# Kernel tuning notes

Measured on AMD Instinct MI355X. Metric: run time of the kernel, lower is better.

## Reference

```python
import jax, jax.numpy as jnp
import numpy as np

N = 50000        # nodes
E = 1_600_000    # edges (avg degree 32)
D_IN = 128
D_H = 128
D_OUT = 128


def expmap0(x):
    # Poincare ball (c=1): expmap0(v) = tanh(||v||) * v / ||v||
    n = jnp.maximum(jnp.linalg.norm(x, axis=-1, keepdims=True), 1e-15)
    return jnp.tanh(n) * x / n


def gat_layer(x, src, dst, W, a_src, a_dst, b, n_nodes):
    # PyG GATConv, heads=1: h = xW; e_ij = LeakyReLU(a_src.h_j + a_dst.h_i);
    # softmax over incoming edges of each target i; out_i = sum_j alpha_ij h_j + b
    h = x @ W                                   # [N, d_out]
    s = h @ a_src                               # [N]
    d = h @ a_dst                               # [N]
    e = jax.nn.leaky_relu(s[src] + d[dst], 0.2)  # [E']
    m = jax.ops.segment_max(e, dst, num_segments=n_nodes)
    num = jnp.exp(e - m[dst])
    den = jax.ops.segment_sum(num, dst, num_segments=n_nodes)
    alpha = num / den[dst]                      # [E']
    out = jax.ops.segment_sum(alpha[:, None] * h[src], dst, num_segments=n_nodes)
    return out + b


def setup_inputs() -> dict:
    key = jax.random.key(0)
    ks = jax.random.split(key, 16)
    p = lambda k, shape: (jax.random.normal(k, shape, jnp.float32) * 0.08)
    inp = {
        "x": jax.random.normal(ks[0], (N, D_IN), jnp.float32),
        "edge_index": jax.random.randint(ks[1], (2, E), 0, N, dtype=jnp.int64)
        if jax.config.jax_enable_x64 else jax.random.randint(ks[1], (2, E), 0, N, dtype=jnp.int32),
        "W1": p(ks[2], (D_IN, D_H)),  "a1s": p(ks[3], (D_H,)), "a1d": p(ks[4], (D_H,)), "b1": jnp.zeros((D_H,), jnp.float32),
        "W2": p(ks[5], (D_H, D_H)),   "a2s": p(ks[6], (D_H,)), "a2d": p(ks[7], (D_H,)), "b2": jnp.zeros((D_H,), jnp.float32),
        "W3": p(ks[8], (D_H, D_OUT)), "a3s": p(ks[9], (D_OUT,)), "a3d": p(ks[10], (D_OUT,)), "b3": jnp.zeros((D_OUT,), jnp.float32),
    }
    return inp


def reference(x, edge_index, W1, a1s, a1d, b1, W2, a2s, a2d, b2, W3, a3s, a3d, b3):
    # add self loops (PyG GATConv default)
    loop = jnp.arange(N, dtype=edge_index.dtype)
    src = jnp.concatenate([edge_index[0], loop])
    dst = jnp.concatenate([edge_index[1], loop])
    h = expmap0(x)
    h = jnp.tanh(gat_layer(h, src, dst, W1, a1s, a1d, b1, N)) * 2
    # dropout(p=0.2) is identity in eval mode
    h = jnp.tanh(gat_layer(h, src, dst, W2, a2s, a2d, b2, N)) * 2
    return gat_layer(h, src, dst, W3, a3s, a3d, b3, N)
```

## Files before the change

kernel.cpp:

```cpp
#include <hip/hip_runtime.h>
#include <math.h>

#define D 128
#define CAP 80

typedef __attribute__((ext_vector_type(8))) short short8;
typedef __attribute__((ext_vector_type(4))) float float4v;
typedef __attribute__((ext_vector_type(4))) _Float16 half4v;

__device__ __forceinline__ unsigned short f2bf(float x) {
    unsigned u = __float_as_uint(x);
    u += ((u >> 16) & 1u) + 0x7fffu;
    return (unsigned short)(u >> 16);
}
__device__ __forceinline__ float bf2f(unsigned short h) {
    return __uint_as_float((unsigned)h << 16);
}


__global__ void k_prep(const float* __restrict__ W0, const float* __restrict__ W1,
                       const float* __restrict__ W2, unsigned short* __restrict__ whi,
                       unsigned short* __restrict__ wlo, int* __restrict__ cnt, int N) {
    int id = blockIdx.x * blockDim.x + threadIdx.x;
    if (id < 6144) {
        int l = id >> 11;
        int id2 = id & 2047;
        const float* W = (l == 0) ? W0 : (l == 1) ? W1 : W2;
        int lane = id2 & 63;
        int tile = id2 >> 6;
        int kt = tile & 3;
        int ct = tile >> 2;
        int k0 = kt * 32 + (lane >> 4) * 8;
        int n  = ct * 16 + (lane & 15);
        size_t base = (size_t)l * 16384 + (size_t)id2 * 8;
        for (int j = 0; j < 8; j++) {
            float w = W[(k0 + j) * D + n];
            unsigned short h = f2bf(w);
            whi[base + j] = h;
            wlo[base + j] = f2bf(w - bf2f(h));
        }
    } else {
        int i = id - 6144;
        if (i < N) cnt[i] = 0;
    }
}


__global__ void k_fill(const int* __restrict__ ei, int E, int N, int* __restrict__ cnt,
                       int* __restrict__ bucket) {
    int part = blockIdx.x & 7;
    int slice = blockIdx.x >> 3;
    int nsl = gridDim.x >> 3;
    int lo = (int)((long long)N * part >> 3);
    int hi = (int)((long long)N * (part + 1) >> 3);
    const int* dst = ei + E;
    for (int i = slice * blockDim.x + threadIdx.x; i < E; i += nsl * blockDim.x) {
        int d_ = dst[i];
        if (d_ >= lo && d_ < hi) {
            int s_ = ei[i];
            int p = atomicAdd(&cnt[d_], 1);
            if (p < CAP) bucket[(size_t)d_ * CAP + p] = s_;
        }
    }
}


template <bool EXP>
__device__ __forceinline__ void prep_frags(const float* __restrict__ A, int rg, int N,
                                           int quad, short8* bhi, short8* blo) {
    bool valid = rg < N;
    const float* arow = &A[(size_t)(valid ? rg : 0) * D];
    float af[32];
#pragma unroll
    for (int kt = 0; kt < 4; kt++) {
        int k0 = kt * 32 + quad * 8;
        float4 x0 = valid ? *(const float4*)&arow[k0]     : make_float4(0.f, 0.f, 0.f, 0.f);
        float4 x1 = valid ? *(const float4*)&arow[k0 + 4] : make_float4(0.f, 0.f, 0.f, 0.f);
        af[kt * 8 + 0] = x0.x; af[kt * 8 + 1] = x0.y; af[kt * 8 + 2] = x0.z; af[kt * 8 + 3] = x0.w;
        af[kt * 8 + 4] = x1.x; af[kt * 8 + 5] = x1.y; af[kt * 8 + 6] = x1.z; af[kt * 8 + 7] = x1.w;
    }
    if (EXP) {
        float ss = 0.f;
#pragma unroll
        for (int q = 0; q < 32; q++) ss += af[q] * af[q];
        ss += __shfl_xor(ss, 16, 64);
        ss += __shfl_xor(ss, 32, 64);
        float n = fmaxf(sqrtf(ss), 1e-15f);
        float sc = tanhf(n) / n;
#pragma unroll
        for (int q = 0; q < 32; q++) af[q] *= sc;
    }
#pragma unroll
    for (int kt = 0; kt < 4; kt++) {
#pragma unroll
        for (int j = 0; j < 8; j++) {
            float v = af[kt * 8 + j];
            unsigned short h = f2bf(v);
            bhi[kt][j] = (short)h;
            blo[kt][j] = (short)f2bf(v - bf2f(h));
        }
    }
}


template <bool EXP>
__global__ __launch_bounds__(256) void k_gemm(const float* __restrict__ A,
                                              const unsigned short* __restrict__ Whi,
                                              const unsigned short* __restrict__ Wlo,
                                              const float* __restrict__ avS,
                                              const float* __restrict__ avD,
                                              _Float16* __restrict__ H,
                                              float* __restrict__ sA,
                                              float* __restrict__ dA, int N) {
    __shared__ unsigned short WshHi[16384];
    __shared__ unsigned short WshLo[16384];
    int t = threadIdx.x;
    int wv = t >> 6, lane = t & 63, quad = lane >> 4, m = lane & 15;

    {
        const uint4* gh = (const uint4*)Whi;
        const uint4* gl = (const uint4*)Wlo;
        uint4* sh = (uint4*)WshHi;
        uint4* sl = (uint4*)WshLo;
#pragma unroll
        for (int i = 0; i < 8; i++) {
            sh[i * 256 + t] = gh[i * 256 + t];
            sl[i * 256 + t] = gl[i * 256 + t];
        }
    }

    int rg = blockIdx.x * 64 + wv * 16 + m;
    short8 bhi[4], blo[4];
    prep_frags<EXP>(A, rg, N, quad, bhi, blo);

    __syncthreads();

    bool valid = rg < N;

    float4v acc[8];
#pragma unroll
    for (int ct = 0; ct < 8; ct++) acc[ct] = (float4v){0.f, 0.f, 0.f, 0.f};

#pragma unroll
    for (int kt = 0; kt < 4; kt++) {
#pragma unroll
        for (int ct = 0; ct < 8; ct++) {
            int wofs = (((ct << 2) | kt) * 64 + lane) * 8;
            short8 whi = *(const short8*)&WshHi[wofs];
            short8 wlo = *(const short8*)&WshLo[wofs];
            acc[ct] = __builtin_amdgcn_mfma_f32_16x16x32_bf16(wlo, blo[kt], acc[ct], 0, 0, 0);
            acc[ct] = __builtin_amdgcn_mfma_f32_16x16x32_bf16(whi, blo[kt], acc[ct], 0, 0, 0);
            acc[ct] = __builtin_amdgcn_mfma_f32_16x16x32_bf16(wlo, bhi[kt], acc[ct], 0, 0, 0);
            acc[ct] = __builtin_amdgcn_mfma_f32_16x16x32_bf16(whi, bhi[kt], acc[ct], 0, 0, 0);
        }
    }

    if (valid) {
#pragma unroll
        for (int ct = 0; ct < 8; ct++) {
            half4v o;
            o[0] = (_Float16)acc[ct][0];
            o[1] = (_Float16)acc[ct][1];
            o[2] = (_Float16)acc[ct][2];
            o[3] = (_Float16)acc[ct][3];
            *(half4v*)&H[(size_t)rg * D + ct * 16 + quad * 4] = o;
        }
    }

    float ps = 0.f, pd = 0.f;
#pragma unroll
    for (int ct = 0; ct < 8; ct++) {
        int fb = ct * 16 + quad * 4;
        float4 as4 = *(const float4*)&avS[fb];
        float4 ad4 = *(const float4*)&avD[fb];
        ps += acc[ct][0] * as4.x + acc[ct][1] * as4.y + acc[ct][2] * as4.z + acc[ct][3] * as4.w;
        pd += acc[ct][0] * ad4.x + acc[ct][1] * ad4.y + acc[ct][2] * ad4.z + acc[ct][3] * ad4.w;
    }
    ps += __shfl_xor(ps, 16, 64);
    ps += __shfl_xor(ps, 32, 64);
    pd += __shfl_xor(pd, 16, 64);
    pd += __shfl_xor(pd, 32, 64);
    if (quad == 0 && valid) {
        sA[rg] = ps;
        dA[rg] = pd;
    }
}


template <bool ACT>
__global__ __launch_bounds__(256) void k_agg(const _Float16* __restrict__ H,
                                             const float* __restrict__ sA,
                                             const float* __restrict__ dA,
                                             const int* __restrict__ cnt,
                                             const int* __restrict__ bucket,
                                             const float* __restrict__ bias,
                                             float* __restrict__ out, int N) {
    int lane = threadIdx.x & 63;
    int node = blockIdx.x * 4 + (threadIdx.x >> 6);
    if (node >= N) return;
    int deg   = __builtin_amdgcn_readfirstlane(cnt[node]);
    if (deg > CAP) deg = CAP;
    int start = node * CAP;
    int end   = start + deg;
    const int* csr = bucket;
    const half4v* Hv = (const half4v*)H;
    float di  = dA[node];
    int half  = lane >> 5;
    int hq    = lane & 31;
    int cq    = hq * 4;

    float ax = 0.f, ay = 0.f, az = 0.f, aw = 0.f;
    float den = 0.f;
    int j = start;

    for (; j + 8 <= end; j += 8) {
        int s0 = csr[j + 0], s1 = csr[j + 1], s2 = csr[j + 2], s3 = csr[j + 3];
        int s4 = csr[j + 4], s5 = csr[j + 5], s6 = csr[j + 6], s7 = csr[j + 7];
        float e0 = sA[s0] + di, e1 = sA[s1] + di, e2 = sA[s2] + di, e3 = sA[s3] + di;
        float e4 = sA[s4] + di, e5 = sA[s5] + di, e6 = sA[s6] + di, e7 = sA[s7] + di;
        e0 = (e0 > 0.f) ? e0 : 0.2f * e0;
        e1 = (e1 > 0.f) ? e1 : 0.2f * e1;
        e2 = (e2 > 0.f) ? e2 : 0.2f * e2;
        e3 = (e3 > 0.f) ? e3 : 0.2f * e3;
        e4 = (e4 > 0.f) ? e4 : 0.2f * e4;
        e5 = (e5 > 0.f) ? e5 : 0.2f * e5;
        e6 = (e6 > 0.f) ? e6 : 0.2f * e6;
        e7 = (e7 > 0.f) ? e7 : 0.2f * e7;
        float p0 = __expf(e0), p1 = __expf(e1), p2 = __expf(e2), p3 = __expf(e3);
        float p4 = __expf(e4), p5 = __expf(e5), p6 = __expf(e6), p7 = __expf(e7);
        int   ra = half ? s1 : s0;
        int   rb = half ? s3 : s2;
        int   rc = half ? s5 : s4;
        int   rd = half ? s7 : s6;
        float wa = half ? p1 : p0;
        float wb = half ? p3 : p2;
        float wc = half ? p5 : p4;
        float wd = half ? p7 : p6;
        half4v ha = Hv[(size_t)ra * 32 + hq];
        half4v hb = Hv[(size_t)rb * 32 + hq];
        half4v hc = Hv[(size_t)rc * 32 + hq];
        half4v hd = Hv[(size_t)rd * 32 + hq];
        den += (wa + wb) + (wc + wd);
        ax += wa * (float)ha[0] + wb * (float)hb[0] + wc * (float)hc[0] + wd * (float)hd[0];
        ay += wa * (float)ha[1] + wb * (float)hb[1] + wc * (float)hc[1] + wd * (float)hd[1];
        az += wa * (float)ha[2] + wb * (float)hb[2] + wc * (float)hc[2] + wd * (float)hd[2];
        aw += wa * (float)ha[3] + wb * (float)hb[3] + wc * (float)hc[3] + wd * (float)hd[3];
    }
    if (j + 4 <= end) {
        int s0 = csr[j + 0], s1 = csr[j + 1], s2 = csr[j + 2], s3 = csr[j + 3];
        float e0 = sA[s0] + di, e1 = sA[s1] + di, e2 = sA[s2] + di, e3 = sA[s3] + di;
        e0 = (e0 > 0.f) ? e0 : 0.2f * e0;
        e1 = (e1 > 0.f) ? e1 : 0.2f * e1;
        e2 = (e2 > 0.f) ? e2 : 0.2f * e2;
        e3 = (e3 > 0.f) ? e3 : 0.2f * e3;
        float p0 = __expf(e0), p1 = __expf(e1), p2 = __expf(e2), p3 = __expf(e3);
        int   ra = half ? s1 : s0;
        int   rb = half ? s3 : s2;
        float wa = half ? p1 : p0;
        float wb = half ? p3 : p2;
        half4v ha = Hv[(size_t)ra * 32 + hq];
        half4v hb = Hv[(size_t)rb * 32 + hq];
        den += wa + wb;
        ax += wa * (float)ha[0] + wb * (float)hb[0];
        ay += wa * (float)ha[1] + wb * (float)hb[1];
        az += wa * (float)ha[2] + wb * (float)hb[2];
        aw += wa * (float)ha[3] + wb * (float)hb[3];
        j += 4;
    }
    if (j + 2 <= end) {
        int s0 = csr[j + 0], s1 = csr[j + 1];
        float e0 = sA[s0] + di, e1 = sA[s1] + di;
        e0 = (e0 > 0.f) ? e0 : 0.2f * e0;
        e1 = (e1 > 0.f) ? e1 : 0.2f * e1;
        float p0 = __expf(e0), p1 = __expf(e1);
        int   ra = half ? s1 : s0;
        float wa = half ? p1 : p0;
        den += wa;
        half4v ha = Hv[(size_t)ra * 32 + hq];
        ax += wa * (float)ha[0]; ay += wa * (float)ha[1];
        az += wa * (float)ha[2]; aw += wa * (float)ha[3];
        j += 2;
    }
    if (j < end && half == 0) {
        int s0 = csr[j];
        float e0 = sA[s0] + di;
        e0 = (e0 > 0.f) ? e0 : 0.2f * e0;
        float p0 = __expf(e0);
        den += p0;
        half4v ha = Hv[(size_t)s0 * 32 + hq];
        ax += p0 * (float)ha[0]; ay += p0 * (float)ha[1];
        az += p0 * (float)ha[2]; aw += p0 * (float)ha[3];
    }

    if (half == 0) {
        float e0 = sA[node] + di;
        e0 = (e0 > 0.f) ? e0 : 0.2f * e0;
        float p0 = __expf(e0);
        den += p0;
        half4v ha = Hv[(size_t)node * 32 + hq];
        ax += p0 * (float)ha[0]; ay += p0 * (float)ha[1];
        az += p0 * (float)ha[2]; aw += p0 * (float)ha[3];
    }

    ax  += __shfl_xor(ax, 32, 64);
    ay  += __shfl_xor(ay, 32, 64);
    az  += __shfl_xor(az, 32, 64);
    aw  += __shfl_xor(aw, 32, 64);
    den += __shfl_xor(den, 32, 64);

    if (half == 0) {
        float iv = 1.f / den;
        float4 b4 = *(const float4*)&bias[cq];
        float vx = ax * iv + b4.x;
        float vy = ay * iv + b4.y;
        float vz = az * iv + b4.z;
        float vw = aw * iv + b4.w;
        if (ACT) {
            vx = 2.f * tanhf(vx);
            vy = 2.f * tanhf(vy);
            vz = 2.f * tanhf(vz);
            vw = 2.f * tanhf(vw);
        }
        *(float4*)&out[(size_t)node * D + cq] = make_float4(vx, vy, vz, vw);
    }
}


extern "C" void kernel_launch(void* const* d_in, const int* in_sizes, int n_in,
                              void* d_out, int out_size, void* d_ws, size_t ws_size,
                              hipStream_t stream) {
    const int N = in_sizes[0] / D;
    const int E = in_sizes[1] / 2;
    const float* x = (const float*)d_in[0];
    const int* ei = (const int*)d_in[1];
    const float* Wm[3] = {(const float*)d_in[2], (const float*)d_in[6], (const float*)d_in[10]};
    const float* aS[3] = {(const float*)d_in[3], (const float*)d_in[7], (const float*)d_in[11]};
    const float* aD[3] = {(const float*)d_in[4], (const float*)d_in[8], (const float*)d_in[12]};
    const float* bb[3] = {(const float*)d_in[5], (const float*)d_in[9], (const float*)d_in[13]};

    char* ws = (char*)d_ws;
    size_t off = 0;
    auto alloc = [&](size_t bytes) -> void* {
        void* p = ws + off;
        off = (off + bytes + 511) & ~(size_t)511;
        return p;
    };
    float*     bufA   = (float*)alloc((size_t)N * D * 4);
    _Float16*  bufB   = (_Float16*)alloc((size_t)N * D * 2);
    float*     sArr   = (float*)alloc((size_t)N * 4);
    float*     dArr   = (float*)alloc((size_t)N * 4);
    int*       cnt    = (int*)alloc((size_t)N * 4);
    int*       bucket = (int*)alloc((size_t)N * CAP * 4);
    unsigned short* whiB = (unsigned short*)alloc((size_t)3 * D * D * 2);
    unsigned short* wloB = (unsigned short*)alloc((size_t)3 * D * D * 2);
    (void)ws_size; (void)n_in; (void)out_size;

    k_prep<<<(6144 + N + 255) / 256, 256, 0, stream>>>(Wm[0], Wm[1], Wm[2],
                                                       whiB, wloB, cnt, N);
    k_fill<<<1024, 256, 0, stream>>>(ei, E, N, cnt, bucket);

    const int gemmBlocks = (N + 63) / 64;
    for (int l = 0; l < 3; l++) {
        const unsigned short* whi = whiB + (size_t)l * 16384;
        const unsigned short* wlo = wloB + (size_t)l * 16384;
        if (l == 0) {
            k_gemm<true><<<gemmBlocks, 256, 0, stream>>>(x, whi, wlo, aS[0], aD[0],
                                                         bufB, sArr, dArr, N);
        } else {
            k_gemm<false><<<gemmBlocks, 256, 0, stream>>>(bufA, whi, wlo, aS[l], aD[l],
                                                          bufB, sArr, dArr, N);
        }
        if (l < 2) {
            k_agg<true><<<(N + 3) / 4, 256, 0, stream>>>(bufB, sArr, dArr, cnt, bucket,
                                                         bb[l], bufA, N);
        } else {
            k_agg<false><<<(N + 3) / 4, 256, 0, stream>>>(bufB, sArr, dArr, cnt, bucket,
                                                          bb[l], (float*)d_out, N);
        }
    }
}
```

Baseline: 413.2 us.

## Pad edge counters to 64-byte stride and flatten bucket fill into one pass

The bucket-fill kernel no longer rescans the whole edge list eight times, once per destination partition. Each thread now loads eight edges with vectorized nontemporal loads and appends them in a single pass. The per-node counters are padded to a 16-int stride so concurrent atomics on neighbouring nodes land on separate cache lines and contend less. In exchange, the counter array grows 16x, which enlarges the zeroing work in the prep kernel and spreads the degree reads in aggregation. The partitioned scan also gave write locality, and dropping it makes bucket writes more scattered.

After: 456.4 us. 10.5% more time.

```diff
diff --git a/kernel.cpp b/kernel.cpp
--- a/kernel.cpp
+++ b/kernel.cpp
@@ -3,10 +3,12 @@
 
 #define D 128
 #define CAP 80
+#define CNTS 16
 
 typedef __attribute__((ext_vector_type(8))) short short8;
 typedef __attribute__((ext_vector_type(4))) float float4v;
 typedef __attribute__((ext_vector_type(4))) _Float16 half4v;
+typedef __attribute__((ext_vector_type(4))) int int4v;
 
 __device__ __forceinline__ unsigned short f2bf(float x) {
     unsigned u = __float_as_uint(x);
@@ -41,24 +43,45 @@
         }
     } else {
         int i = id - 6144;
-        if (i < N) cnt[i] = 0;
-    }
-}
-
-
-__global__ void k_fill(const int* __restrict__ ei, int E, int N, int* __restrict__ cnt,
-                       int* __restrict__ bucket) {
-    int part = blockIdx.x & 7;
-    int slice = blockIdx.x >> 3;
-    int nsl = gridDim.x >> 3;
-    int lo = (int)((long long)N * part >> 3);
-    int hi = (int)((long long)N * (part + 1) >> 3);
-    const int* dst = ei + E;
-    for (int i = slice * blockDim.x + threadIdx.x; i < E; i += nsl * blockDim.x) {
-        int d_ = dst[i];
-        if (d_ >= lo && d_ < hi) {
-            int s_ = ei[i];
-            int p = atomicAdd(&cnt[d_], 1);
+        if (i < N * CNTS) cnt[i] = 0;
+    }
+}
+
+
+__global__ __launch_bounds__(256) void k_fill(const int* __restrict__ ei, int E,
+                                              int* __restrict__ cnt,
+                                              int* __restrict__ bucket) {
+    int i = blockIdx.x * 256 + threadIdx.x;
+    int base = i << 3;
+    if (base >= E) return;
+    const int* srcp = ei;
+    const int* dstp = ei + E;
+    if (base + 8 <= E) {
+        int4v d0 = __builtin_nontemporal_load((const int4v*)&dstp[base]);
+        int4v d1 = __builtin_nontemporal_load((const int4v*)&dstp[base + 4]);
+        int4v s0 = __builtin_nontemporal_load((const int4v*)&srcp[base]);
+        int4v s1 = __builtin_nontemporal_load((const int4v*)&srcp[base + 4]);
+        int p0 = atomicAdd(&cnt[d0.x << 4], 1);
+        int p1 = atomicAdd(&cnt[d0.y << 4], 1);
+        int p2 = atomicAdd(&cnt[d0.z << 4], 1);
+        int p3 = atomicAdd(&cnt[d0.w << 4], 1);
+        int p4 = atomicAdd(&cnt[d1.x << 4], 1);
+        int p5 = atomicAdd(&cnt[d1.y << 4], 1);
+        int p6 = atomicAdd(&cnt[d1.z << 4], 1);
+        int p7 = atomicAdd(&cnt[d1.w << 4], 1);
+        if (p0 < CAP) bucket[(size_t)d0.x * CAP + p0] = s0.x;
+        if (p1 < CAP) bucket[(size_t)d0.y * CAP + p1] = s0.y;
+        if (p2 < CAP) bucket[(size_t)d0.z * CAP + p2] = s0.z;
+        if (p3 < CAP) bucket[(size_t)d0.w * CAP + p3] = s0.w;
+        if (p4 < CAP) bucket[(size_t)d1.x * CAP + p4] = s1.x;
+        if (p5 < CAP) bucket[(size_t)d1.y * CAP + p5] = s1.y;
+        if (p6 < CAP) bucket[(size_t)d1.z * CAP + p6] = s1.z;
+        if (p7 < CAP) bucket[(size_t)d1.w * CAP + p7] = s1.w;
+    } else {
+        for (int e = base; e < E; e++) {
+            int d_ = dstp[e];
+            int s_ = srcp[e];
+            int p = atomicAdd(&cnt[d_ << 4], 1);
             if (p < CAP) bucket[(size_t)d_ * CAP + p] = s_;
         }
     }
@@ -198,7 +221,7 @@
     int lane = threadIdx.x & 63;
     int node = blockIdx.x * 4 + (threadIdx.x >> 6);
     if (node >= N) return;
-    int deg   = __builtin_amdgcn_readfirstlane(cnt[node]);
+    int deg   = __builtin_amdgcn_readfirstlane(cnt[node << 4]);
     if (deg > CAP) deg = CAP;
     int start = node * CAP;
     int end   = start + deg;
@@ -349,15 +372,16 @@
     _Float16*  bufB   = (_Float16*)alloc((size_t)N * D * 2);
     float*     sArr   = (float*)alloc((size_t)N * 4);
     float*     dArr   = (float*)alloc((size_t)N * 4);
-    int*       cnt    = (int*)alloc((size_t)N * 4);
+    int*       cnt    = (int*)alloc((size_t)N * CNTS * 4);
     int*       bucket = (int*)alloc((size_t)N * CAP * 4);
     unsigned short* whiB = (unsigned short*)alloc((size_t)3 * D * D * 2);
     unsigned short* wloB = (unsigned short*)alloc((size_t)3 * D * D * 2);
     (void)ws_size; (void)n_in; (void)out_size;
 
-    k_prep<<<(6144 + N + 255) / 256, 256, 0, stream>>>(Wm[0], Wm[1], Wm[2],
-                                                       whiB, wloB, cnt, N);
-    k_fill<<<1024, 256, 0, stream>>>(ei, E, N, cnt, bucket);
+    k_prep<<<(6144 + N * CNTS + 255) / 256, 256, 0, stream>>>(Wm[0], Wm[1], Wm[2],
+                                                              whiB, wloB, cnt, N);
+    const int fillThreads = (E + 7) / 8;
+    k_fill<<<(fillThreads + 255) / 256, 256, 0, stream>>>(ei, E, cnt, bucket);
 
     const int gemmBlocks = (N + 63) / 64;
     for (int l = 0; l < 3; l++) {
```
